# Kernel optimization log

Hardware: AMD Instinct MI355X
Metric: run time of the kernel (lower is better)

The kernel has to match this reference:

```python
import jax, jax.numpy as jnp
import numpy as np

I = 256   # input_size
H = 512   # hidden_size
B = 8192  # batch


def setup_inputs() -> dict:
    key = jax.random.key(0)
    ks = jax.random.split(key, 16)
    def rn(k, shape, scale):
        return (jax.random.normal(k, shape, dtype=jnp.float32) * scale)
    inp = {
        "x": rn(ks[0], (B, I), 1.0),
        "h": rn(ks[1], (B, H), 0.1),
        "c": rn(ks[2], (B, H), 0.1),
        # attention MLP: Linear(I+H -> I), Linear(I -> I)
        "aw0": rn(ks[3], (I, I + H), (I + H) ** -0.5),
        "ab0": rn(ks[4], (I,), 0.01),
        "aw1": rn(ks[5], (I, I), I ** -0.5),
        "ab1": rn(ks[6], (I,), 0.01),
        # LSTMCell params, PyTorch layout: [4H, I] / [4H, H], gate order i,f,g,o
        "w_ih": rn(ks[7], (4 * H, I), I ** -0.5),
        "b_ih": rn(ks[8], (4 * H,), 0.01),
        "w_hh": rn(ks[9], (4 * H, H), H ** -0.5),
        "b_hh": rn(ks[10], (4 * H,), 0.01),
        # output head: Linear(H -> H), Linear(H -> 1)
        "ow0": rn(ks[11], (H, H), H ** -0.5),
        "ob0": rn(ks[12], (H,), 0.01),
        "ow1": rn(ks[13], (1, H), H ** -0.5),
        "ob1": rn(ks[14], (1,), 0.01),
    }
    return inp


def reference(x, h, c, aw0, ab0, aw1, ab1, w_ih, b_ih, w_hh, b_hh, ow0, ob0, ow1, ob1):
    # attention gate over the input features
    xh = jnp.concatenate([x, h], axis=1)                    # [B, I+H]
    a0 = jax.nn.relu(xh @ aw0.T + ab0)                      # [B, I]
    logits = a0 @ aw1.T + ab1                               # [B, I]
    attn = jax.nn.softmax(logits, axis=1)                   # attention == 1
    x_att = x * attn                                        # [B, I]

    # LSTMCell (torch gate order: i, f, g, o)
    gates = x_att @ w_ih.T + b_ih + h @ w_hh.T + b_hh       # [B, 4H]
    i_g, f_g, g_g, o_g = jnp.split(gates, 4, axis=1)
    i_g = jax.nn.sigmoid(i_g)
    f_g = jax.nn.sigmoid(f_g)
    g_g = jnp.tanh(g_g)
    o_g = jax.nn.sigmoid(o_g)
    c_new = f_g * c + i_g * g_g
    h_new = o_g * jnp.tanh(c_new)

    # 2-layer MLP head -> sigmoid scalar per row
    out = jax.nn.relu(h_new @ ow0.T + ob0)                  # [B, H]
    out = jax.nn.sigmoid(out @ ow1.T + ob1)                 # [B, 1]
    return (out, h_new, c_new, attn)
```

## Files before the change

### kernel.cpp

```cpp
#include <hip/hip_runtime.h>
#include <hip/hip_bf16.h>

#define BROWS 8192
#define IDIM 256
#define HDIM 512
#define KCAT 768
#define G4 2048

typedef __bf16 bf16_t;
typedef bf16_t bf16x8 __attribute__((ext_vector_type(8)));
typedef float f32x4 __attribute__((ext_vector_type(4)));

__device__ __forceinline__ f32x4 mfma16(bf16x8 a, bf16x8 b, f32x4 c) {
    return __builtin_amdgcn_mfma_f32_16x16x32_bf16(a, b, c, 0, 0, 0);
}

__device__ __forceinline__ ushort f2bf(float f) {
    union { float f; unsigned u; } v; v.f = f;
    unsigned u = v.u;
    unsigned r = (u + 0x7fffu + ((u >> 16) & 1u)) >> 16;
    return (ushort)r;
}

__device__ __forceinline__ float bf2f(ushort u) {
    union { unsigned u; float f; } v; v.u = (unsigned)u << 16; return v.f;
}

__device__ __forceinline__ float sigmoidf_(float x) {
    return 1.f / (1.f + __expf(-x));
}
__device__ __forceinline__ float tanhf_(float x) {
    return 1.f - 2.f / (__expf(2.f * x) + 1.f);
}

typedef __attribute__((address_space(1))) const unsigned gas_u32;
typedef __attribute__((address_space(3))) unsigned las_u32;
__device__ __forceinline__ void gld_lds16(const void* g, void* l) {
    __builtin_amdgcn_global_load_lds((gas_u32*)g, (las_u32*)l, 16, 0, 0);
}

__global__ void __launch_bounds__(256) prep_kernel(
        const float* __restrict__ x, const float* __restrict__ h,
        const float* __restrict__ aw0, const float* __restrict__ aw1,
        const float* __restrict__ w_ih, const float* __restrict__ w_hh,
        const float* __restrict__ ow0,
        ushort* __restrict__ xh, ushort* __restrict__ baw0,
        ushort* __restrict__ baw1, ushort* __restrict__ wcat,
        ushort* __restrict__ bow0) {
    int idx = (blockIdx.x * 256 + threadIdx.x) * 4;
    const int N_XH = BROWS * KCAT;
    const int N_AW0 = IDIM * KCAT;
    const int N_AW1 = IDIM * IDIM;
    const int N_WCAT = G4 * KCAT;
    const int N_OW0 = HDIM * HDIM;
    float4 v;
    ushort* dst;
    if (idx < N_XH) {
        int b = idx / KCAT, k = idx - b * KCAT;
        v = (k < IDIM) ? *(const float4*)&x[b * IDIM + k]
                       : *(const float4*)&h[b * HDIM + (k - IDIM)];
        dst = &xh[idx];
    } else if ((idx -= N_XH) < N_AW0) {
        v = *(const float4*)&aw0[idx]; dst = &baw0[idx];
    } else if ((idx -= N_AW0) < N_AW1) {
        v = *(const float4*)&aw1[idx]; dst = &baw1[idx];
    } else if ((idx -= N_AW1) < N_WCAT) {
        int o = idx / KCAT, k = idx - o * KCAT;
        v = (k < IDIM) ? *(const float4*)&w_ih[o * IDIM + k]
                       : *(const float4*)&w_hh[o * HDIM + (k - IDIM)];
        dst = &wcat[idx];
    } else if ((idx -= N_WCAT) < N_OW0) {
        v = *(const float4*)&ow0[idx]; dst = &bow0[idx];
    } else {
        return;
    }
    ushort4 o4 = { f2bf(v.x), f2bf(v.y), f2bf(v.z), f2bf(v.w) };
    *(ushort4*)dst = o4;
}

template<int RELU_BF16>
__global__ void __launch_bounds__(512, 4) staged_gemm(
        const ushort* __restrict__ A, const ushort* __restrict__ W,
        const float* __restrict__ bias, void* __restrict__ outp,
        int Kdim, int out_ld) {
    __shared__ ushort As[2][4096];
    __shared__ ushort Ws[2][2048];
    const int tid = threadIdx.x;
    const int lane = tid & 63, wave = tid >> 6;
    const int wm = wave >> 1, wn = wave & 1;
    const int r = lane & 15, g = lane >> 4;
    const int rb = blockIdx.x & 63, cb = blockIdx.x >> 6;
    const int row0 = rb * 128, col0 = cb * 64;
    const int rl = lane >> 2, chq = lane & 3;
    const int s_sw = (chq ^ ((rl >> 1) & 3)) * 8;
    const int rsw = (g ^ ((r >> 1) & 3)) * 8;
    const bool doW = wave < 4;

    const ushort* aP = A + (size_t)(row0 + wave * 16 + rl) * Kdim + s_sw;
    const ushort* wP = W + (size_t)(col0 + (wave & 3) * 16 + rl) * Kdim + s_sw;

    f32x4 acc[2][2] = {};

    auto stage = [&](int buf, int t) {
        const int o = t * 32;
        gld_lds16(aP + o, &As[buf][wave * 512]);
        if (doW) gld_lds16(wP + o, &Ws[buf][(wave & 3) * 512]);
    };
    auto compute = [&](int buf) {
        bf16x8 af[2], wf[2];
#pragma unroll
        for (int m = 0; m < 2; m++)
            af[m] = *(const bf16x8*)&As[buf][(wm * 2 + m) * 512 + r * 32 + rsw];
#pragma unroll
        for (int n = 0; n < 2; n++)
            wf[n] = *(const bf16x8*)&Ws[buf][(wn * 2 + n) * 512 + r * 32 + rsw];
#pragma unroll
        for (int m = 0; m < 2; m++)
#pragma unroll
            for (int n = 0; n < 2; n++)
                acc[m][n] = mfma16(af[m], wf[n], acc[m][n]);
    };

    stage(0, 0);
    const int NT = Kdim >> 5;
    int cur = 0;
    for (int t = 0; t < NT; t++) {
        __builtin_amdgcn_s_barrier();
        if (t + 1 < NT) {
            stage(cur ^ 1, t + 1);
            if (doW) asm volatile("s_waitcnt vmcnt(2)" ::: "memory");
            else     asm volatile("s_waitcnt vmcnt(1)" ::: "memory");
        } else {
            asm volatile("s_waitcnt vmcnt(0)" ::: "memory");
        }
        __builtin_amdgcn_s_barrier();
        compute(cur);
        cur ^= 1;
    }

#pragma unroll
    for (int n = 0; n < 2; n++) {
        int col = col0 + wn * 32 + n * 16 + r;
        float bv = bias[col];
#pragma unroll
        for (int m = 0; m < 2; m++) {
            int rbase = row0 + wm * 32 + m * 16 + g * 4;
#pragma unroll
            for (int reg = 0; reg < 4; reg++) {
                float v = acc[m][n][reg] + bv;
                if (RELU_BF16) {
                    v = v > 0.f ? v : 0.f;
                    ((ushort*)outp)[(size_t)(rbase + reg) * out_ld + col] = f2bf(v);
                } else {
                    ((float*)outp)[(size_t)(rbase + reg) * out_ld + col] = v;
                }
            }
        }
    }
}

__global__ void __launch_bounds__(256) attn_softmax(
        const float* __restrict__ logits, const float* __restrict__ x,
        float* __restrict__ attn_out, ushort* __restrict__ xh) {
    const int wave = threadIdx.x >> 6, lane = threadIdx.x & 63;
    const int row = blockIdx.x * 4 + wave;
    float v[4];
    float m = -1e30f;
#pragma unroll
    for (int i = 0; i < 4; i++) {
        v[i] = logits[row * IDIM + i * 64 + lane];
        m = fmaxf(m, v[i]);
    }
#pragma unroll
    for (int s = 32; s; s >>= 1) m = fmaxf(m, __shfl_xor(m, s, 64));
    float sum = 0.f;
#pragma unroll
    for (int i = 0; i < 4; i++) { v[i] = __expf(v[i] - m); sum += v[i]; }
#pragma unroll
    for (int s = 32; s; s >>= 1) sum += __shfl_xor(sum, s, 64);
    float inv = 1.f / sum;
#pragma unroll
    for (int i = 0; i < 4; i++) {
        int idx = i * 64 + lane;
        float a = v[i] * inv;
        attn_out[row * IDIM + idx] = a;
        xh[row * KCAT + idx] = f2bf(x[row * IDIM + idx] * a);
    }
}

__global__ void __launch_bounds__(1024, 4) gates_staged(
        const ushort* __restrict__ A, const ushort* __restrict__ W,
        const float* __restrict__ b_ih, const float* __restrict__ b_hh,
        const float* __restrict__ c_in,
        float* __restrict__ h_out, float* __restrict__ c_out,
        ushort* __restrict__ h_bf) {
    __shared__ ushort As[2 * 8192];
    __shared__ ushort Ws[2 * 8192];
    const int tid = threadIdx.x;
    const int lane = tid & 63, wave = tid >> 6;
    const int wm = wave >> 2, wn = wave & 3;
    const int r = lane & 15, g = lane >> 4;
    const int bid = blockIdx.x;
    const int xcd = bid & 7, local = bid >> 3;
    const int rb = xcd * 4 + (local & 3);
    const int cb = local >> 2;
    const int row0 = rb * 256;
    const int j0 = cb * 64;
    const int rl = lane >> 2, chq = lane & 3;
    const int s_sw = (chq ^ ((rl >> 1) & 3)) * 8;
    const int rsw = (g ^ ((r >> 1) & 3)) * 8;

    auto wrow = [&](int cc) {
        return ((cc >> 4) & 3) * HDIM + j0 + (cc & 15) + ((cc >> 6) << 4);
    };
    const ushort* aP = A + (size_t)(row0 + wave * 16 + rl) * KCAT + s_sw;
    const ushort* wP = W + (size_t)wrow(wave * 16 + rl) * KCAT + s_sw;

    f32x4 acc[4][4] = {};

    auto stage = [&](int buf, int t) {
        const int o = t * 32;
        gld_lds16(aP + o, &As[buf * 8192 + wave * 512]);
        gld_lds16(wP + o, &Ws[buf * 8192 + wave * 512]);
    };
    auto compute = [&](int buf) {
        bf16x8 af[4], wf[4];
#pragma unroll
        for (int m = 0; m < 4; m++)
            af[m] = *(const bf16x8*)&As[buf * 8192 + (wm * 4 + m) * 512 + r * 32 + rsw];
#pragma unroll
        for (int n = 0; n < 4; n++)
            wf[n] = *(const bf16x8*)&Ws[buf * 8192 + (wn * 4 + n) * 512 + r * 32 + rsw];
#pragma unroll
        for (int m = 0; m < 4; m++)
#pragma unroll
            for (int n = 0; n < 4; n++)
                acc[m][n] = mfma16(af[m], wf[n], acc[m][n]);
    };

    stage(0, 0);
    const int NT = KCAT >> 5;
    int cur = 0;
    for (int t = 0; t < NT; t++) {
        __builtin_amdgcn_s_barrier();
        if (t + 1 < NT) {
            stage(cur ^ 1, t + 1);
            asm volatile("s_waitcnt vmcnt(2)" ::: "memory");
        } else {
            asm volatile("s_waitcnt vmcnt(0)" ::: "memory");
        }
        __builtin_amdgcn_s_barrier();
        compute(cur);
        cur ^= 1;
    }

    const int j = j0 + wn * 16 + r;
    float bb[4];
#pragma unroll
    for (int n = 0; n < 4; n++) bb[n] = b_ih[n * HDIM + j] + b_hh[n * HDIM + j];
#pragma unroll
    for (int m = 0; m < 4; m++) {
        int rbase = row0 + wm * 64 + m * 16 + g * 4;
#pragma unroll
        for (int reg = 0; reg < 4; reg++) {
            int row = rbase + reg;
            float ig = sigmoidf_(acc[m][0][reg] + bb[0]);
            float fg = sigmoidf_(acc[m][1][reg] + bb[1]);
            float gg = tanhf_(acc[m][2][reg] + bb[2]);
            float og = sigmoidf_(acc[m][3][reg] + bb[3]);
            float cn = fg * c_in[(size_t)row * HDIM + j] + ig * gg;
            float hn = og * tanhf_(cn);
            c_out[(size_t)row * HDIM + j] = cn;
            h_out[(size_t)row * HDIM + j] = hn;
            h_bf[(size_t)row * HDIM + j] = f2bf(hn);
        }
    }
}

__global__ void __launch_bounds__(256) head_gemv(
        const ushort* __restrict__ Hrelu, const float* __restrict__ ow1,
        const float* __restrict__ ob1, float* __restrict__ outp) {
    const int wave = threadIdx.x >> 6, lane = threadIdx.x & 63;
    const int row = blockIdx.x * 4 + wave;
    typedef ushort u16x8 __attribute__((ext_vector_type(8)));
    u16x8 hv = *(const u16x8*)&Hrelu[(size_t)row * HDIM + lane * 8];
    float4 w0 = *(const float4*)&ow1[lane * 8];
    float4 w1 = *(const float4*)&ow1[lane * 8 + 4];
    float s = bf2f(hv[0]) * w0.x + bf2f(hv[1]) * w0.y + bf2f(hv[2]) * w0.z +
              bf2f(hv[3]) * w0.w + bf2f(hv[4]) * w1.x + bf2f(hv[5]) * w1.y +
              bf2f(hv[6]) * w1.z + bf2f(hv[7]) * w1.w;
#pragma unroll
    for (int sh = 32; sh; sh >>= 1) s += __shfl_xor(s, sh, 64);
    if (lane == 0) outp[row] = 1.f / (1.f + __expf(-(s + ob1[0])));
}

extern "C" void kernel_launch(void* const* d_in, const int* in_sizes, int n_in,
                              void* d_out, int out_size, void* d_ws, size_t ws_size,
                              hipStream_t stream) {
    const float* x    = (const float*)d_in[0];
    const float* h    = (const float*)d_in[1];
    const float* c    = (const float*)d_in[2];
    const float* aw0  = (const float*)d_in[3];
    const float* ab0  = (const float*)d_in[4];
    const float* aw1  = (const float*)d_in[5];
    const float* ab1  = (const float*)d_in[6];
    const float* w_ih = (const float*)d_in[7];
    const float* b_ih = (const float*)d_in[8];
    const float* w_hh = (const float*)d_in[9];
    const float* b_hh = (const float*)d_in[10];
    const float* ow0  = (const float*)d_in[11];
    const float* ob0  = (const float*)d_in[12];
    const float* ow1  = (const float*)d_in[13];
    const float* ob1  = (const float*)d_in[14];

    char* ws = (char*)d_ws;
    ushort* xh     = (ushort*)(ws + 0);
    ushort* a0     = (ushort*)(ws + 12582912);
    float*  logits = (float*) (ws + 16777216);
    ushort* hrelu  = (ushort*)(ws + 16777216);
    ushort* hbf    = (ushort*)(ws + 25165824);
    ushort* baw0   = (ushort*)(ws + 33554432);
    ushort* baw1   = (ushort*)(ws + 33947648);
    ushort* wcat   = (ushort*)(ws + 34078720);
    ushort* bow0   = (ushort*)(ws + 37224448);

    float* outv    = (float*)d_out;
    float* h_out   = outv + 8192;
    float* c_out   = outv + 4202496;
    float* attn_o  = outv + 8396800;

    prep_kernel<<<8192, 256, 0, stream>>>(x, h, aw0, aw1, w_ih, w_hh, ow0,
                                          xh, baw0, baw1, wcat, bow0);
    staged_gemm<1><<<256, 512, 0, stream>>>(xh, baw0, ab0, a0, KCAT, IDIM);
    staged_gemm<0><<<256, 512, 0, stream>>>(a0, baw1, ab1, logits, IDIM, IDIM);
    attn_softmax<<<2048, 256, 0, stream>>>(logits, x, attn_o, xh);
    gates_staged<<<256, 1024, 0, stream>>>(xh, wcat, b_ih, b_hh, c,
                                           h_out, c_out, hbf);
    staged_gemm<1><<<512, 512, 0, stream>>>(hbf, bow0, ob0, hrelu, HDIM, HDIM);
    head_gemv<<<2048, 256, 0, stream>>>(hrelu, ow1, ob1, outv);
}
```

Measured before the change: 89.12 us.

## Fuse second attention GEMM with softmax and x scaling in one kernel

Replaces the separate logits GEMM and the row-softmax kernel with one kernel. Each 512-thread block computes a 32x256 logits tile with MFMA from double-buffered LDS, writes it to shared memory and then runs the softmax and the x*attn bf16 conversion in place. This removes the fp32 logits round trip through global memory and one kernel launch. In exchange each block covers only 32 rows with the full 256-column weight slice, so weight reuse per block is lower and LDS use is higher.

```diff
diff --git a/kernel.cpp b/kernel.cpp
--- a/kernel.cpp
+++ b/kernel.cpp
@@ -159,32 +159,99 @@
     }
 }
 
-__global__ void __launch_bounds__(256) attn_softmax(
-        const float* __restrict__ logits, const float* __restrict__ x,
+__global__ void __launch_bounds__(512) logits_softmax(
+        const ushort* __restrict__ A, const ushort* __restrict__ W,
+        const float* __restrict__ bias, const float* __restrict__ x,
         float* __restrict__ attn_out, ushort* __restrict__ xh) {
-    const int wave = threadIdx.x >> 6, lane = threadIdx.x & 63;
-    const int row = blockIdx.x * 4 + wave;
-    float v[4];
-    float m = -1e30f;
+    __shared__ ushort As[2][1024];
+    __shared__ ushort Ws[2][8192];
+    __shared__ float lg[32][264];
+    const int tid = threadIdx.x;
+    const int lane = tid & 63, wave = tid >> 6;
+    const int wm = wave >> 2, wn = wave & 3;
+    const int r = lane & 15, g = lane >> 4;
+    const int row0 = blockIdx.x * 32;
+    const int rl = lane >> 2, chq = lane & 3;
+    const int s_sw = (chq ^ ((rl >> 1) & 3)) * 8;
+    const int rsw = (g ^ ((r >> 1) & 3)) * 8;
+    const bool doA = wave < 2;
+
+    const ushort* aP  = A + (size_t)(row0 + wave * 16 + rl) * IDIM + s_sw;
+    const ushort* wP0 = W + (size_t)(wave * 32 + rl) * IDIM + s_sw;
+    const ushort* wP1 = W + (size_t)(wave * 32 + 16 + rl) * IDIM + s_sw;
+
+    f32x4 acc[4] = {};
+
+    auto stage = [&](int buf, int t) {
+        const int o = t * 32;
+        if (doA) gld_lds16(aP + o, &As[buf][wave * 512]);
+        gld_lds16(wP0 + o, &Ws[buf][(2 * wave) * 512]);
+        gld_lds16(wP1 + o, &Ws[buf][(2 * wave + 1) * 512]);
+    };
+    auto compute = [&](int buf) {
+        bf16x8 af = *(const bf16x8*)&As[buf][wm * 512 + r * 32 + rsw];
+        bf16x8 wf[4];
+#pragma unroll
+        for (int n = 0; n < 4; n++)
+            wf[n] = *(const bf16x8*)&Ws[buf][(wn * 4 + n) * 512 + r * 32 + rsw];
+#pragma unroll
+        for (int n = 0; n < 4; n++)
+            acc[n] = mfma16(af, wf[n], acc[n]);
+    };
+
+    stage(0, 0);
+    const int NT = IDIM >> 5;
+    int cur = 0;
+    for (int t = 0; t < NT; t++) {
+        __builtin_amdgcn_s_barrier();
+        if (t + 1 < NT) {
+            stage(cur ^ 1, t + 1);
+            if (doA) asm volatile("s_waitcnt vmcnt(3)" ::: "memory");
+            else     asm volatile("s_waitcnt vmcnt(2)" ::: "memory");
+        } else {
+            asm volatile("s_waitcnt vmcnt(0)" ::: "memory");
+        }
+        __builtin_amdgcn_s_barrier();
+        compute(cur);
+        cur ^= 1;
+    }
+
+#pragma unroll
+    for (int n = 0; n < 4; n++) {
+        int col = wn * 64 + n * 16 + r;
+        float bv = bias[col];
+#pragma unroll
+        for (int reg = 0; reg < 4; reg++)
+            lg[wm * 16 + g * 4 + reg][col] = acc[n][reg] + bv;
+    }
+    __syncthreads();
+
 #pragma unroll
     for (int i = 0; i < 4; i++) {
-        v[i] = logits[row * IDIM + i * 64 + lane];
-        m = fmaxf(m, v[i]);
-    }
-#pragma unroll
-    for (int s = 32; s; s >>= 1) m = fmaxf(m, __shfl_xor(m, s, 64));
-    float sum = 0.f;
-#pragma unroll
-    for (int i = 0; i < 4; i++) { v[i] = __expf(v[i] - m); sum += v[i]; }
-#pragma unroll
-    for (int s = 32; s; s >>= 1) sum += __shfl_xor(sum, s, 64);
-    float inv = 1.f / sum;
-#pragma unroll
-    for (int i = 0; i < 4; i++) {
-        int idx = i * 64 + lane;
-        float a = v[i] * inv;
-        attn_out[row * IDIM + idx] = a;
-        xh[row * KCAT + idx] = f2bf(x[row * IDIM + idx] * a);
+        const int rr = wave * 4 + i;
+        const int grow = row0 + rr;
+        float v[4];
+        float m = -1e30f;
+#pragma unroll
+        for (int j = 0; j < 4; j++) {
+            v[j] = lg[rr][j * 64 + lane];
+            m = fmaxf(m, v[j]);
+        }
+#pragma unroll
+        for (int s = 32; s; s >>= 1) m = fmaxf(m, __shfl_xor(m, s, 64));
+        float sum = 0.f;
+#pragma unroll
+        for (int j = 0; j < 4; j++) { v[j] = __expf(v[j] - m); sum += v[j]; }
+#pragma unroll
+        for (int s = 32; s; s >>= 1) sum += __shfl_xor(sum, s, 64);
+        float inv = 1.f / sum;
+#pragma unroll
+        for (int j = 0; j < 4; j++) {
+            int idx = j * 64 + lane;
+            float a = v[j] * inv;
+            attn_out[(size_t)grow * IDIM + idx] = a;
+            xh[(size_t)grow * KCAT + idx] = f2bf(x[(size_t)grow * IDIM + idx] * a);
+        }
     }
 }
 
@@ -316,7 +383,6 @@
     char* ws = (char*)d_ws;
     ushort* xh     = (ushort*)(ws + 0);
     ushort* a0     = (ushort*)(ws + 12582912);
-    float*  logits = (float*) (ws + 16777216);
     ushort* hrelu  = (ushort*)(ws + 16777216);
     ushort* hbf    = (ushort*)(ws + 25165824);
     ushort* baw0   = (ushort*)(ws + 33554432);
@@ -332,8 +398,7 @@
     prep_kernel<<<8192, 256, 0, stream>>>(x, h, aw0, aw1, w_ih, w_hh, ow0,
                                           xh, baw0, baw1, wcat, bow0);
     staged_gemm<1><<<256, 512, 0, stream>>>(xh, baw0, ab0, a0, KCAT, IDIM);
-    staged_gemm<0><<<256, 512, 0, stream>>>(a0, baw1, ab1, logits, IDIM, IDIM);
-    attn_softmax<<<2048, 256, 0, stream>>>(logits, x, attn_o, xh);
+    logits_softmax<<<256, 512, 0, stream>>>(a0, baw1, ab1, x, attn_o, xh);
     gates_staged<<<256, 1024, 0, stream>>>(xh, wcat, b_ih, b_hh, c,
                                            h_out, c_out, hbf);
     staged_gemm<1><<<512, 512, 0, stream>>>(hbf, bow0, ob0, hrelu, HDIM, HDIM);
```

New measurement: 86.03 us, median of 2. -3.5%, faster.
